# Optimization experiments

Measured on AMD Instinct MI355X. Metric: run time of the kernel, lower is better.

The kernel has to match this reference:

```python
import jax, jax.numpy as jnp
import numpy as np

K, N = 4, 128
NODEDIM = 256
EDGEDIM_IN = 256
EDGEDIM_OUT = 256
GLOBALDIM = 256
INFODIM = 2 * NODEDIM + GLOBALDIM + EDGEDIM_IN  # 1024


def setup_inputs() -> dict:
    key = jax.random.key(0)
    ks = jax.random.split(key, 10)
    u = jax.random.normal(ks[0], (K, GLOBALDIM), dtype=jnp.float32)
    h_v = jax.random.normal(ks[1], (K, N, NODEDIM), dtype=jnp.float32)
    h_e = jax.random.normal(ks[2], (K, N, N, EDGEDIM_IN), dtype=jnp.float32)
    V = jax.random.randint(ks[3], (K, N), 0, 2).astype(jnp.float32)  # binary node mask
    E = jax.random.randint(ks[4], (K, N, N, 2), 0, 2, dtype=jnp.int32)  # per-type edge mask
    # function[1] params (loop runs i in [1, num_functions) -> only i=1)
    s1 = 1.0 / np.sqrt(INFODIM)
    W1 = jax.random.uniform(ks[5], (INFODIM, INFODIM), jnp.float32, -s1, s1)
    b1 = jax.random.uniform(ks[6], (INFODIM,), jnp.float32, -s1, s1)
    W2 = jax.random.uniform(ks[7], (INFODIM, EDGEDIM_OUT), jnp.float32, -s1, s1)
    b2 = jax.random.uniform(ks[8], (EDGEDIM_OUT,), jnp.float32, -s1, s1)
    return {"u": u, "h_v": h_v, "h_e": h_e, "V": V, "E": E,
            "W1": W1, "b1": b1, "W2": W2, "b2": b2}


def reference(u, h_v, h_e, V, E, W1, b1, W2, b2):
    Kb, Nn = h_v.shape[0], h_v.shape[1]
    hv = h_v * V[..., None]                                    # masked node states
    src = jnp.broadcast_to(hv[:, :, None, :], (Kb, Nn, Nn, NODEDIM))
    tgt = jnp.broadcast_to(hv[:, None, :, :], (Kb, Nn, Nn, NODEDIM))
    glb = jnp.broadcast_to(u[:, None, None, :], (Kb, Nn, Nn, GLOBALDIM))
    edge_feat = jnp.concatenate([src, tgt, glb, h_e], axis=-1)  # [K,N,N,INFODIM]
    # per-type MLP (only function index 1 executes for num_functions=2)
    h = jax.nn.elu(jnp.einsum('knmi,ij->knmj', edge_feat, W1) + b1)
    out = jnp.einsum('knmi,io->knmo', h, W2) + b2               # [K,N,N,EDGEDIM_OUT]
    mask = (E[..., 1] == 1)[..., None]
    h_e_update = jnp.where(mask, out, jnp.zeros((), out.dtype))
    # residual=True, history=True
    return h_e_update + h_e
```

## Files before the change

### kernel.cpp

```cpp
#include <hip/hip_runtime.h>
#include <stdint.h>

#define DEVI __device__ __forceinline__

typedef short bf16x8 __attribute__((ext_vector_type(8)));
typedef float f32x4  __attribute__((ext_vector_type(4)));

DEVI short f2bf(float f){
  union { float f; uint32_t u; } un; un.f = f;
  uint32_t u = un.u;
  u += 0x7fffu + ((u >> 16) & 1u);
  return (short)(u >> 16);
}
DEVI float bf2f(uint32_t us){
  union { uint32_t u; float f; } x; x.u = us << 16; return x.f;
}

DEVI f32x4 mfma16(bf16x8 a, bf16x8 b, f32x4 c){
  return __builtin_amdgcn_mfma_f32_16x16x32_bf16(a, b, c, 0, 0, 0);
}

__global__ __launch_bounds__(256) void prep_all(
    const float* __restrict__ W1, const float* __restrict__ W2,
    const float* __restrict__ hv, const float* __restrict__ V,
    const float* __restrict__ u,
    short* __restrict__ w1t, short* __restrict__ w2t,
    short* __restrict__ hvb, short* __restrict__ ub)
{
  const int bid = blockIdx.x;
  if (bid < 1280){
    const float* W = (bid < 1024) ? W1 : W2;
    short* WT      = (bid < 1024) ? w1t : w2t;
    const int R = 1024;
    const int C = (bid < 1024) ? 1024 : 256;
    const int b2 = (bid < 1024) ? bid : (bid - 1024);
    __shared__ float tile[32][33];
    int ctiles = C >> 5;
    int bi = b2 / ctiles, bj = b2 % ctiles;
    int tx = threadIdx.x & 31, ty = threadIdx.x >> 5;
    #pragma unroll
    for (int r = 0; r < 4; ++r){
      int i = bi*32 + ty + r*8;
      tile[ty + r*8][tx] = W[(size_t)i*C + bj*32 + tx];
    }
    __syncthreads();
    #pragma unroll
    for (int r = 0; r < 4; ++r){
      int j = bj*32 + ty + r*8;
      WT[(size_t)j*R + bi*32 + tx] = f2bf(tile[tx][ty + r*8]);
    }
  } else {
    int idx = (bid - 1280)*256 + threadIdx.x;
    if (idx < 512*256){
      int r = idx >> 8;
      hvb[idx] = f2bf(hv[idx] * V[r]);
    } else if (idx < 512*256 + 1024){
      int i2 = idx - 512*256;
      ub[i2] = f2bf(u[i2]);
    }
  }
}

__global__ __launch_bounds__(256) void prep_st(
    const short* __restrict__ hvb, const short* __restrict__ ub,
    const short* __restrict__ w1t, const float* __restrict__ b1,
    short* __restrict__ sbuf, short* __restrict__ tbuf)
{
  const int bid = blockIdx.x;
  const int st = bid >> 7;
  const int rt8 = (bid >> 4) & 7;
  const int ctile = bid & 15;
  const int r0 = rt8 << 6, j0 = ctile << 6;
  const int tid = threadIdx.x;
  const int w = tid >> 6, l = tid & 63;
  const int l15 = l & 15, l4 = l >> 4;
  __shared__ short A[64*256];
  __shared__ short Stile[64][64];
  for (int q = 0; q < 8; ++q){
    int id = tid + (q << 8);
    int row = id >> 5, c8 = id & 31;
    bf16x8 v = *(const bf16x8*)(hvb + (size_t)(r0 + row)*256 + c8*8);
    *(bf16x8*)((char*)A + row*512 + ((c8*16) ^ ((row & 7) << 4))) = v;
  }
  __syncthreads();
  const int wr = w >> 1, wc = w & 1;
  const int rowbase = wr << 5, colbase = wc << 5;
  const int swzA = (l15 & 7) << 4;
  f32x4 acc[2][2];
  acc[0][0]=0; acc[0][1]=0; acc[1][0]=0; acc[1][1]=0;
  const int ioff = st ? 256 : 0;
  const short* w1p = w1t + (size_t)(j0 + colbase + l15)*1024 + ioff + l4*8;
  const char* ap0 = (const char*)A + (rowbase + l15)*512;
  const char* ap1 = ap0 + 16*512;
  #pragma unroll
  for (int kk = 0; kk < 8; ++kk){
    int ib = kk*64 + l4*16;
    bf16x8 a0 = *(const bf16x8*)(ap0 + (ib ^ swzA));
    bf16x8 a1 = *(const bf16x8*)(ap1 + (ib ^ swzA));
    bf16x8 b0 = *(const bf16x8*)(w1p + kk*32);
    bf16x8 b1v = *(const bf16x8*)(w1p + 16*1024 + kk*32);
    acc[0][0] = mfma16(a0, b0, acc[0][0]);
    acc[1][0] = mfma16(a1, b0, acc[1][0]);
    acc[0][1] = mfma16(a0, b1v, acc[0][1]);
    acc[1][1] = mfma16(a1, b1v, acc[1][1]);
  }
  if (st == 0){
    const int kb = r0 >> 7;
    const short* up = ub + kb*256 + l4*8;
    const short* w1pu = w1t + (size_t)(j0 + colbase + l15)*1024 + 512 + l4*8;
    #pragma unroll
    for (int kk = 0; kk < 8; ++kk){
      bf16x8 au = *(const bf16x8*)(up + kk*32);
      bf16x8 b0 = *(const bf16x8*)(w1pu + kk*32);
      bf16x8 b1v = *(const bf16x8*)(w1pu + 16*1024 + kk*32);
      acc[0][0] = mfma16(au, b0, acc[0][0]);
      acc[1][0] = mfma16(au, b0, acc[1][0]);
      acc[0][1] = mfma16(au, b1v, acc[0][1]);
      acc[1][1] = mfma16(au, b1v, acc[1][1]);
    }
  }
  #pragma unroll
  for (int r = 0; r < 2; ++r){
    #pragma unroll
    for (int c = 0; c < 2; ++c){
      int jl = colbase + c*16 + l15;
      float badd = st ? 0.f : b1[j0 + jl];
      #pragma unroll
      for (int reg = 0; reg < 4; ++reg){
        int rowl = rowbase + r*16 + l4*4 + reg;
        short v = f2bf(acc[r][c][reg] + badd);
        if (st == 0) Stile[rowl][jl] = v;
        else         Stile[jl][rowl] = v;
      }
    }
  }
  __syncthreads();
  {
    int a = tid >> 2, ch = (tid & 3) << 4;
    bf16x8 v0 = *(const bf16x8*)(&Stile[a][ch]);
    bf16x8 v1 = *(const bf16x8*)(&Stile[a][ch + 8]);
    short* dst = (st == 0)
      ? (sbuf + (size_t)(r0 + a)*1024 + j0 + ch)
      : (tbuf + (size_t)(j0 + a)*512  + r0 + ch);
    *(bf16x8*)(dst)     = v0;
    *(bf16x8*)(dst + 8) = v1;
  }
}

__global__ __launch_bounds__(512, 2) void fused_edge(
    const float* __restrict__ he, const unsigned short* __restrict__ sb,
    const unsigned short* __restrict__ tbT, const short* __restrict__ w1t,
    const short* __restrict__ w2t, const float* __restrict__ b2,
    const int* __restrict__ Em, float* __restrict__ out)
{
  const int bo = blockIdx.x;
  const int b = ((bo & 7) << 6) | (bo >> 3);
  const int kp = b >> 8;
  const int n  = (b >> 1) & 127;
  const int m0 = (b & 1) << 6;
  const int k0 = kp << 1;
  const int tid = threadIdx.x;
  const int w = tid >> 6, l = tid & 63;
  const int l15 = l & 15, l4 = l >> 4;

  __shared__ short heb[128*256];
  __shared__ short eluv[2][128*128];
  __shared__ int   emask[128];

  const int base0 = (k0*128 + n)*128 + m0;

  #pragma unroll
  for (int q = 0; q < 8; ++q){
    int id = tid + (q << 9);
    int row = id >> 5, c8 = id & 31;
    size_t grow = (size_t)base0 + (row >> 6)*16384 + (row & 63);
    const float4* p = (const float4*)(he + grow*256 + c8*8);
    float4 a4 = p[0], b4 = p[1];
    union { bf16x8 v; short s[8]; } pk;
    pk.s[0]=f2bf(a4.x); pk.s[1]=f2bf(a4.y); pk.s[2]=f2bf(a4.z); pk.s[3]=f2bf(a4.w);
    pk.s[4]=f2bf(b4.x); pk.s[5]=f2bf(b4.y); pk.s[6]=f2bf(b4.z); pk.s[7]=f2bf(b4.w);
    *(bf16x8*)((char*)heb + row*512 + ((c8*16) ^ ((row & 7) << 4))) = pk.v;
  }
  if (tid < 128)
    emask[tid] = Em[((size_t)base0 + (tid >> 6)*16384 + (tid & 63))*2 + 1];
  __syncthreads();

  f32x4 acc2[8][2];
  #pragma unroll
  for (int i = 0; i < 8; ++i){ acc2[i][0] = 0; acc2[i][1] = 0; }

  const unsigned short* srow0 = sb + (size_t)(k0*128 + n)*1024;
  const unsigned short* srow1 = srow0 + 128*1024;
  const int tcol0 = k0*128 + m0;
  const int tcol1 = tcol0 + 128;
  const char* hb = (const char*)heb;
  const int swz = (l15 & 7) << 4;

  union u4 { ushort4 v; unsigned short s[4]; };

  bf16x8 bw1[8];
  {
    const short* w1p = w1t + (size_t)(w*16 + l15)*1024 + 768 + l4*8;
    #pragma unroll
    for (int kk = 0; kk < 8; ++kk) bw1[kk] = *(const bf16x8*)(w1p + kk*32);
  }
  u4 t4[8];
  #pragma unroll
  for (int rt = 0; rt < 8; ++rt){
    int tc = (rt < 4) ? (tcol0 + rt*16) : (tcol1 + (rt - 4)*16);
    t4[rt].v = *(const ushort4*)(tbT + (size_t)(w*16 + l15)*512 + tc + l4*4);
  }
  float sv0 = bf2f(srow0[w*16 + l15]);
  float sv1 = bf2f(srow1[w*16 + l15]);

  for (int ph = 0; ph < 8; ++ph){
    const int jcol = ph*128 + w*16 + l15;

    f32x4 acc1[8];
    #pragma unroll
    for (int i = 0; i < 8; ++i) acc1[i] = 0;
    #pragma unroll
    for (int kk = 0; kk < 8; ++kk){
      int ib = kk*64 + l4*16;
      #pragma unroll
      for (int rt = 0; rt < 8; ++rt){
        int row = rt*16 + l15;
        bf16x8 a = *(const bf16x8*)(hb + row*512 + (ib ^ swz));
        acc1[rt] = mfma16(a, bw1[kk], acc1[rt]);
      }
    }

    const short* w2p = w2t + (size_t)(w*32 + l15)*1024 + ph*128 + l4*8;
    bf16x8 bw2[2][4];
    #pragma unroll
    for (int ct = 0; ct < 2; ++ct)
      #pragma unroll
      for (int kk = 0; kk < 4; ++kk)
        bw2[ct][kk] = *(const bf16x8*)(w2p + (size_t)ct*16*1024 + kk*32);

    if (ph < 7){
      const short* w1p = w1t + (size_t)(jcol + 128)*1024 + 768 + l4*8;
      #pragma unroll
      for (int kk = 0; kk < 8; ++kk) bw1[kk] = *(const bf16x8*)(w1p + kk*32);
    }

    char* eb = (char*)(&eluv[ph & 1][0]);
    const int cb = (w*16 + l15)*2;
    #pragma unroll
    for (int rt = 0; rt < 8; ++rt){
      float sv = (rt < 4) ? sv0 : sv1;
      #pragma unroll
      for (int reg = 0; reg < 4; ++reg){
        int row = rt*16 + l4*4 + reg;
        float v = acc1[rt][reg] + sv + bf2f(t4[rt].s[reg]);
        v = v > 0.f ? v : (__expf(v) - 1.f);
        *(short*)(eb + row*256 + (cb ^ ((row & 7) << 4))) = f2bf(v);
      }
    }

    if (ph < 7){
      #pragma unroll
      for (int rt = 0; rt < 8; ++rt){
        int tc = (rt < 4) ? (tcol0 + rt*16) : (tcol1 + (rt - 4)*16);
        t4[rt].v = *(const ushort4*)(tbT + (size_t)(jcol + 128)*512 + tc + l4*4);
      }
      sv0 = bf2f(srow0[jcol + 128]);
      sv1 = bf2f(srow1[jcol + 128]);
    }
    __syncthreads();

    #pragma unroll
    for (int kk = 0; kk < 4; ++kk){
      int jb = kk*64 + l4*16;
      #pragma unroll
      for (int rt = 0; rt < 8; ++rt){
        int row = rt*16 + l15;
        bf16x8 a2 = *(const bf16x8*)(eb + row*256 + (jb ^ ((row & 7) << 4)));
        acc2[rt][0] = mfma16(a2, bw2[0][kk], acc2[rt][0]);
        acc2[rt][1] = mfma16(a2, bw2[1][kk], acc2[rt][1]);
      }
    }
  }

  const float bias0 = b2[w*32 + l15];
  const float bias1 = b2[w*32 + 16 + l15];
  #pragma unroll
  for (int rt = 0; rt < 8; ++rt){
    #pragma unroll
    for (int reg = 0; reg < 4; ++reg){
      int row = rt*16 + l4*4 + reg;
      int e = emask[row];
      size_t grow = (size_t)base0 + (row >> 6)*16384 + (row & 63);
      float* op = out + grow*256 + w*32 + l15;
      const char* hrow = hb + row*512;
      int sw = (row & 7) << 4;
      float hv0 = bf2f(*(const unsigned short*)(hrow + (((w*32 + l15)*2) ^ sw)));
      float hv1 = bf2f(*(const unsigned short*)(hrow + (((w*32 + 16 + l15)*2) ^ sw)));
      op[0]  = ((e == 1) ? (acc2[rt][0][reg] + bias0) : 0.f) + hv0;
      op[16] = ((e == 1) ? (acc2[rt][1][reg] + bias1) : 0.f) + hv1;
    }
  }
}

extern "C" void kernel_launch(void* const* d_in, const int* in_sizes, int n_in,
                              void* d_out, int out_size, void* d_ws, size_t ws_size,
                              hipStream_t stream)
{
  const float* u   = (const float*)d_in[0];
  const float* h_v = (const float*)d_in[1];
  const float* h_e = (const float*)d_in[2];
  const float* V   = (const float*)d_in[3];
  const int*   E   = (const int*)d_in[4];
  const float* W1  = (const float*)d_in[5];
  const float* b1  = (const float*)d_in[6];
  const float* W2  = (const float*)d_in[7];
  const float* b2  = (const float*)d_in[8];
  float* out = (float*)d_out;

  char* ws = (char*)d_ws;
  short* w1t  = (short*)(ws);
  short* w2t  = (short*)(ws + (2u<<20));
  short* hvb  = (short*)(ws + (2u<<20) + (512u<<10));
  short* ub   = (short*)(ws + (2u<<20) + (768u<<10));
  short* sbuf = (short*)(ws + (3u<<20));
  short* tbuf = (short*)(ws + (4u<<20));

  prep_all<<<1796, 256, 0, stream>>>(W1, W2, h_v, V, u, w1t, w2t, hvb, ub);
  prep_st<<<256, 256, 0, stream>>>(hvb, ub, w1t, b1, sbuf, tbuf);
  fused_edge<<<512, 512, 0, stream>>>(h_e,
                                      (const unsigned short*)sbuf,
                                      (const unsigned short*)tbuf,
                                      w1t, w2t, b2, E, out);
}
```

Measured before the change: 177.0 us.

## Process two hidden column tiles per phase with single ELU buffer

Each warp now computes two 16-column slices of the first GEMM per phase (256 hidden columns), so every LDS read of the edge-feature A fragment feeds two MFMAs, and the phase count halves from 8 to 4. The double-buffered ELU tile is replaced by a single 128x256 buffer with an extra barrier before it is overwritten. Weight fragments are now loaded inside the k-loop instead of being prefetched a phase ahead. Register pressure roughly doubles for the layer-1 accumulators, which risks spills under the 512x2 launch bounds, and the second barrier plus the loss of weight prefetch may expose load latency.

```diff
diff --git a/kernel.cpp b/kernel.cpp
--- a/kernel.cpp
+++ b/kernel.cpp
@@ -164,7 +164,7 @@
   const int l15 = l & 15, l4 = l >> 4;
 
   __shared__ short heb[128*256];
-  __shared__ short eluv[2][128*128];
+  __shared__ short eluv[128*256];
   __shared__ int   emask[128];
 
   const int base0 = (k0*128 + n)*128 + m0;
@@ -194,90 +194,94 @@
   const int tcol0 = k0*128 + m0;
   const int tcol1 = tcol0 + 128;
   const char* hb = (const char*)heb;
+  const char* eb = (const char*)eluv;
   const int swz = (l15 & 7) << 4;
 
   union u4 { ushort4 v; unsigned short s[4]; };
 
-  bf16x8 bw1[8];
-  {
-    const short* w1p = w1t + (size_t)(w*16 + l15)*1024 + 768 + l4*8;
-    #pragma unroll
-    for (int kk = 0; kk < 8; ++kk) bw1[kk] = *(const bf16x8*)(w1p + kk*32);
-  }
-  u4 t4[8];
+  u4 t4a[8], t4b[8];
   #pragma unroll
   for (int rt = 0; rt < 8; ++rt){
     int tc = (rt < 4) ? (tcol0 + rt*16) : (tcol1 + (rt - 4)*16);
-    t4[rt].v = *(const ushort4*)(tbT + (size_t)(w*16 + l15)*512 + tc + l4*4);
-  }
-  float sv0 = bf2f(srow0[w*16 + l15]);
-  float sv1 = bf2f(srow1[w*16 + l15]);
-
-  for (int ph = 0; ph < 8; ++ph){
-    const int jcol = ph*128 + w*16 + l15;
-
-    f32x4 acc1[8];
-    #pragma unroll
-    for (int i = 0; i < 8; ++i) acc1[i] = 0;
-    #pragma unroll
-    for (int kk = 0; kk < 8; ++kk){
-      int ib = kk*64 + l4*16;
-      #pragma unroll
-      for (int rt = 0; rt < 8; ++rt){
-        int row = rt*16 + l15;
-        bf16x8 a = *(const bf16x8*)(hb + row*512 + (ib ^ swz));
-        acc1[rt] = mfma16(a, bw1[kk], acc1[rt]);
-      }
-    }
-
-    const short* w2p = w2t + (size_t)(w*32 + l15)*1024 + ph*128 + l4*8;
-    bf16x8 bw2[2][4];
-    #pragma unroll
-    for (int ct = 0; ct < 2; ++ct)
-      #pragma unroll
-      for (int kk = 0; kk < 4; ++kk)
-        bw2[ct][kk] = *(const bf16x8*)(w2p + (size_t)ct*16*1024 + kk*32);
-
-    if (ph < 7){
-      const short* w1p = w1t + (size_t)(jcol + 128)*1024 + 768 + l4*8;
-      #pragma unroll
-      for (int kk = 0; kk < 8; ++kk) bw1[kk] = *(const bf16x8*)(w1p + kk*32);
-    }
-
-    char* eb = (char*)(&eluv[ph & 1][0]);
-    const int cb = (w*16 + l15)*2;
+    t4a[rt].v = *(const ushort4*)(tbT + (size_t)(w*16 + l15)*512       + tc + l4*4);
+    t4b[rt].v = *(const ushort4*)(tbT + (size_t)(w*16 + l15 + 128)*512 + tc + l4*4);
+  }
+  float sva0 = bf2f(srow0[w*16 + l15]),       sva1 = bf2f(srow1[w*16 + l15]);
+  float svb0 = bf2f(srow0[w*16 + l15 + 128]), svb1 = bf2f(srow1[w*16 + l15 + 128]);
+
+  for (int ph = 0; ph < 4; ++ph){
+    const int jca = ph*256 + w*16 + l15;
+    const int jcb = jca + 128;
+
+    f32x4 acc1a[8], acc1b[8];
+    #pragma unroll
+    for (int i = 0; i < 8; ++i){ acc1a[i] = 0; acc1b[i] = 0; }
+    {
+      const short* wpa = w1t + (size_t)jca*1024 + 768 + l4*8;
+      const short* wpb = w1t + (size_t)jcb*1024 + 768 + l4*8;
+      #pragma unroll
+      for (int kk = 0; kk < 8; ++kk){
+        bf16x8 ba = *(const bf16x8*)(wpa + kk*32);
+        bf16x8 bb = *(const bf16x8*)(wpb + kk*32);
+        int ib = kk*64 + l4*16;
+        #pragma unroll
+        for (int rt = 0; rt < 8; ++rt){
+          int row = rt*16 + l15;
+          bf16x8 a = *(const bf16x8*)(hb + row*512 + (ib ^ swz));
+          acc1a[rt] = mfma16(a, ba, acc1a[rt]);
+          acc1b[rt] = mfma16(a, bb, acc1b[rt]);
+        }
+      }
+    }
+
+    __syncthreads();
+
+    const int cba = (w*16 + l15)*2;
+    const int cbb = cba + 256;
     #pragma unroll
     for (int rt = 0; rt < 8; ++rt){
-      float sv = (rt < 4) ? sv0 : sv1;
+      float sa = (rt < 4) ? sva0 : sva1;
+      float sbv = (rt < 4) ? svb0 : svb1;
       #pragma unroll
       for (int reg = 0; reg < 4; ++reg){
         int row = rt*16 + l4*4 + reg;
-        float v = acc1[rt][reg] + sv + bf2f(t4[rt].s[reg]);
-        v = v > 0.f ? v : (__expf(v) - 1.f);
-        *(short*)(eb + row*256 + (cb ^ ((row & 7) << 4))) = f2bf(v);
-      }
-    }
-
-    if (ph < 7){
+        int sw = (row & 7) << 4;
+        float va = acc1a[rt][reg] + sa + bf2f(t4a[rt].s[reg]);
+        float vb = acc1b[rt][reg] + sbv + bf2f(t4b[rt].s[reg]);
+        va = va > 0.f ? va : (__expf(va) - 1.f);
+        vb = vb > 0.f ? vb : (__expf(vb) - 1.f);
+        *(short*)((char*)eluv + row*512 + (cba ^ sw)) = f2bf(va);
+        *(short*)((char*)eluv + row*512 + (cbb ^ sw)) = f2bf(vb);
+      }
+    }
+
+    if (ph < 3){
       #pragma unroll
       for (int rt = 0; rt < 8; ++rt){
         int tc = (rt < 4) ? (tcol0 + rt*16) : (tcol1 + (rt - 4)*16);
-        t4[rt].v = *(const ushort4*)(tbT + (size_t)(jcol + 128)*512 + tc + l4*4);
-      }
-      sv0 = bf2f(srow0[jcol + 128]);
-      sv1 = bf2f(srow1[jcol + 128]);
+        t4a[rt].v = *(const ushort4*)(tbT + (size_t)(jca + 256)*512 + tc + l4*4);
+        t4b[rt].v = *(const ushort4*)(tbT + (size_t)(jcb + 256)*512 + tc + l4*4);
+      }
+      sva0 = bf2f(srow0[jca + 256]); sva1 = bf2f(srow1[jca + 256]);
+      svb0 = bf2f(srow0[jcb + 256]); svb1 = bf2f(srow1[jcb + 256]);
     }
     __syncthreads();
 
-    #pragma unroll
-    for (int kk = 0; kk < 4; ++kk){
-      int jb = kk*64 + l4*16;
-      #pragma unroll
-      for (int rt = 0; rt < 8; ++rt){
-        int row = rt*16 + l15;
-        bf16x8 a2 = *(const bf16x8*)(eb + row*256 + (jb ^ ((row & 7) << 4)));
-        acc2[rt][0] = mfma16(a2, bw2[0][kk], acc2[rt][0]);
-        acc2[rt][1] = mfma16(a2, bw2[1][kk], acc2[rt][1]);
+    {
+      const short* wpa = w2t + (size_t)(w*32 + l15)*1024      + ph*256 + l4*8;
+      const short* wpb = w2t + (size_t)(w*32 + 16 + l15)*1024 + ph*256 + l4*8;
+      #pragma unroll
+      for (int kk = 0; kk < 8; ++kk){
+        bf16x8 ba = *(const bf16x8*)(wpa + kk*32);
+        bf16x8 bb = *(const bf16x8*)(wpb + kk*32);
+        int jb = kk*64 + l4*16;
+        #pragma unroll
+        for (int rt = 0; rt < 8; ++rt){
+          int row = rt*16 + l15;
+          bf16x8 a2 = *(const bf16x8*)(eb + row*512 + (jb ^ swz));
+          acc2[rt][0] = mfma16(a2, ba, acc2[rt][0]);
+          acc2[rt][1] = mfma16(a2, bb, acc2[rt][1]);
+        }
       }
     }
   }
```

Result: slower. 209.1 us (+18.1%).

## Retile first GEMM warps to 64x32 blocks for A-fragment reuse

Applied to the files above, without the earlier changes.

Changes the per-warp tiling of the first GEMM from 128 rows by 16 columns to 64 rows by 32 columns, so each LDS A-fragment load feeds two MFMAs. Each warp now handles a single k-batch half, which removes the per-tile selection between two srow/tcol sources. The goal is to halve the LDS reads per MFMA in the hidden-layer GEMM. In exchange each warp holds twice as many W1 fragments in registers.

```diff
diff --git a/kernel.cpp b/kernel.cpp
--- a/kernel.cpp
+++ b/kernel.cpp
@@ -189,44 +189,50 @@
   #pragma unroll
   for (int i = 0; i < 8; ++i){ acc2[i][0] = 0; acc2[i][1] = 0; }
 
-  const unsigned short* srow0 = sb + (size_t)(k0*128 + n)*1024;
-  const unsigned short* srow1 = srow0 + 128*1024;
-  const int tcol0 = k0*128 + m0;
-  const int tcol1 = tcol0 + 128;
+  const int rowbase = (w & 1) << 6;
+  const int colg    = (w >> 1) << 5;
+  const int myk     = w & 1;
+  const unsigned short* srow = sb + (size_t)((k0 + myk)*128 + n)*1024;
+  const int tcol = (k0 + myk)*128 + m0;
   const char* hb = (const char*)heb;
   const int swz = (l15 & 7) << 4;
 
   union u4 { ushort4 v; unsigned short s[4]; };
 
-  bf16x8 bw1[8];
+  bf16x8 bw1a[8], bw1b[8];
   {
-    const short* w1p = w1t + (size_t)(w*16 + l15)*1024 + 768 + l4*8;
-    #pragma unroll
-    for (int kk = 0; kk < 8; ++kk) bw1[kk] = *(const bf16x8*)(w1p + kk*32);
-  }
-  u4 t4[8];
-  #pragma unroll
-  for (int rt = 0; rt < 8; ++rt){
-    int tc = (rt < 4) ? (tcol0 + rt*16) : (tcol1 + (rt - 4)*16);
-    t4[rt].v = *(const ushort4*)(tbT + (size_t)(w*16 + l15)*512 + tc + l4*4);
-  }
-  float sv0 = bf2f(srow0[w*16 + l15]);
-  float sv1 = bf2f(srow1[w*16 + l15]);
+    const short* w1pa = w1t + (size_t)(colg + l15)*1024 + 768 + l4*8;
+    #pragma unroll
+    for (int kk = 0; kk < 8; ++kk){
+      bw1a[kk] = *(const bf16x8*)(w1pa + kk*32);
+      bw1b[kk] = *(const bf16x8*)(w1pa + 16*1024 + kk*32);
+    }
+  }
+  u4 t4a[4], t4b[4];
+  #pragma unroll
+  for (int rt = 0; rt < 4; ++rt){
+    t4a[rt].v = *(const ushort4*)(tbT + (size_t)(colg + l15)*512      + tcol + rt*16 + l4*4);
+    t4b[rt].v = *(const ushort4*)(tbT + (size_t)(colg + 16 + l15)*512 + tcol + rt*16 + l4*4);
+  }
+  float sva = bf2f(srow[colg + l15]);
+  float svb = bf2f(srow[colg + 16 + l15]);
 
   for (int ph = 0; ph < 8; ++ph){
-    const int jcol = ph*128 + w*16 + l15;
-
-    f32x4 acc1[8];
-    #pragma unroll
-    for (int i = 0; i < 8; ++i) acc1[i] = 0;
+    const int jca = ph*128 + colg + l15;
+
+    f32x4 acc1[4][2];
+    #pragma unroll
+    for (int i = 0; i < 4; ++i){ acc1[i][0] = 0; acc1[i][1] = 0; }
     #pragma unroll
     for (int kk = 0; kk < 8; ++kk){
       int ib = kk*64 + l4*16;
-      #pragma unroll
-      for (int rt = 0; rt < 8; ++rt){
-        int row = rt*16 + l15;
+      bf16x8 ba = bw1a[kk], bb = bw1b[kk];
+      #pragma unroll
+      for (int rt = 0; rt < 4; ++rt){
+        int row = rowbase + rt*16 + l15;
         bf16x8 a = *(const bf16x8*)(hb + row*512 + (ib ^ swz));
-        acc1[rt] = mfma16(a, bw1[kk], acc1[rt]);
+        acc1[rt][0] = mfma16(a, ba, acc1[rt][0]);
+        acc1[rt][1] = mfma16(a, bb, acc1[rt][1]);
       }
     }
 
@@ -239,33 +245,39 @@
         bw2[ct][kk] = *(const bf16x8*)(w2p + (size_t)ct*16*1024 + kk*32);
 
     if (ph < 7){
-      const short* w1p = w1t + (size_t)(jcol + 128)*1024 + 768 + l4*8;
-      #pragma unroll
-      for (int kk = 0; kk < 8; ++kk) bw1[kk] = *(const bf16x8*)(w1p + kk*32);
+      const short* w1pa = w1t + (size_t)(jca + 128)*1024 + 768 + l4*8;
+      #pragma unroll
+      for (int kk = 0; kk < 8; ++kk){
+        bw1a[kk] = *(const bf16x8*)(w1pa + kk*32);
+        bw1b[kk] = *(const bf16x8*)(w1pa + 16*1024 + kk*32);
+      }
     }
 
     char* eb = (char*)(&eluv[ph & 1][0]);
-    const int cb = (w*16 + l15)*2;
-    #pragma unroll
-    for (int rt = 0; rt < 8; ++rt){
-      float sv = (rt < 4) ? sv0 : sv1;
+    const int cba = (colg + l15)*2;
+    #pragma unroll
+    for (int rt = 0; rt < 4; ++rt){
       #pragma unroll
       for (int reg = 0; reg < 4; ++reg){
-        int row = rt*16 + l4*4 + reg;
-        float v = acc1[rt][reg] + sv + bf2f(t4[rt].s[reg]);
-        v = v > 0.f ? v : (__expf(v) - 1.f);
-        *(short*)(eb + row*256 + (cb ^ ((row & 7) << 4))) = f2bf(v);
+        int row = rowbase + rt*16 + l4*4 + reg;
+        int sw = (row & 7) << 4;
+        float va = acc1[rt][0][reg] + sva + bf2f(t4a[rt].s[reg]);
+        float vb = acc1[rt][1][reg] + svb + bf2f(t4b[rt].s[reg]);
+        va = va > 0.f ? va : (__expf(va) - 1.f);
+        vb = vb > 0.f ? vb : (__expf(vb) - 1.f);
+        *(short*)(eb + row*256 + (cba ^ sw))        = f2bf(va);
+        *(short*)(eb + row*256 + ((cba + 32) ^ sw)) = f2bf(vb);
       }
     }
 
     if (ph < 7){
       #pragma unroll
-      for (int rt = 0; rt < 8; ++rt){
-        int tc = (rt < 4) ? (tcol0 + rt*16) : (tcol1 + (rt - 4)*16);
-        t4[rt].v = *(const ushort4*)(tbT + (size_t)(jcol + 128)*512 + tc + l4*4);
-      }
-      sv0 = bf2f(srow0[jcol + 128]);
-      sv1 = bf2f(srow1[jcol + 128]);
+      for (int rt = 0; rt < 4; ++rt){
+        t4a[rt].v = *(const ushort4*)(tbT + (size_t)(jca + 128)*512      + tcol + rt*16 + l4*4);
+        t4b[rt].v = *(const ushort4*)(tbT + (size_t)(jca + 16 + 128)*512 + tcol + rt*16 + l4*4);
+      }
+      sva = bf2f(srow[jca + 128]);
+      svb = bf2f(srow[jca + 16 + 128]);
     }
     __syncthreads();
 
```

Measured after the change: 220.8 us. +24.7%, slower.

## Double fused_edge block to 1024 threads and split work across 16 waves

Applied to the files above, without the earlier changes.

The fused edge kernel now runs 16 waves per block instead of 8. In the first GEMM each wave handles a 16-column group for half the rows, one k-slice each. In the second GEMM each wave owns 16 output columns instead of 32. The goal is more waves per CU to hide memory and LDS latency, since the LDS footprint already limits residency to one block per CU. In exchange, pairs of waves load the same W1 fragments, and the launch_bounds(1024,4) setting may force a very tight register budget, which could cause spills.

```diff
diff --git a/kernel.cpp b/kernel.cpp
--- a/kernel.cpp
+++ b/kernel.cpp
@@ -147,7 +147,7 @@
   }
 }
 
-__global__ __launch_bounds__(512, 2) void fused_edge(
+__global__ __launch_bounds__(1024, 4) void fused_edge(
     const float* __restrict__ he, const unsigned short* __restrict__ sb,
     const unsigned short* __restrict__ tbT, const short* __restrict__ w1t,
     const short* __restrict__ w2t, const float* __restrict__ b2,
@@ -170,8 +170,8 @@
   const int base0 = (k0*128 + n)*128 + m0;
 
   #pragma unroll
-  for (int q = 0; q < 8; ++q){
-    int id = tid + (q << 9);
+  for (int q = 0; q < 4; ++q){
+    int id = tid + (q << 10);
     int row = id >> 5, c8 = id & 31;
     size_t grow = (size_t)base0 + (row >> 6)*16384 + (row & 63);
     const float4* p = (const float4*)(he + grow*256 + c8*8);
@@ -185,14 +185,15 @@
     emask[tid] = Em[((size_t)base0 + (tid >> 6)*16384 + (tid & 63))*2 + 1];
   __syncthreads();
 
-  f32x4 acc2[8][2];
-  #pragma unroll
-  for (int i = 0; i < 8; ++i){ acc2[i][0] = 0; acc2[i][1] = 0; }
-
-  const unsigned short* srow0 = sb + (size_t)(k0*128 + n)*1024;
-  const unsigned short* srow1 = srow0 + 128*1024;
-  const int tcol0 = k0*128 + m0;
-  const int tcol1 = tcol0 + 128;
+  f32x4 acc2[8];
+  #pragma unroll
+  for (int i = 0; i < 8; ++i) acc2[i] = 0;
+
+  const int rowbase = (w & 1) << 6;
+  const int colg    = (w >> 1) << 4;
+  const int myk     = w & 1;
+  const unsigned short* srow = sb + (size_t)((k0 + myk)*128 + n)*1024;
+  const int tcol = (k0 + myk)*128 + m0;
   const char* hb = (const char*)heb;
   const int swz = (l15 & 7) << 4;
 
@@ -200,43 +201,37 @@
 
   bf16x8 bw1[8];
   {
-    const short* w1p = w1t + (size_t)(w*16 + l15)*1024 + 768 + l4*8;
+    const short* w1p = w1t + (size_t)(colg + l15)*1024 + 768 + l4*8;
     #pragma unroll
     for (int kk = 0; kk < 8; ++kk) bw1[kk] = *(const bf16x8*)(w1p + kk*32);
   }
-  u4 t4[8];
-  #pragma unroll
-  for (int rt = 0; rt < 8; ++rt){
-    int tc = (rt < 4) ? (tcol0 + rt*16) : (tcol1 + (rt - 4)*16);
-    t4[rt].v = *(const ushort4*)(tbT + (size_t)(w*16 + l15)*512 + tc + l4*4);
-  }
-  float sv0 = bf2f(srow0[w*16 + l15]);
-  float sv1 = bf2f(srow1[w*16 + l15]);
+  u4 t4[4];
+  #pragma unroll
+  for (int rt = 0; rt < 4; ++rt)
+    t4[rt].v = *(const ushort4*)(tbT + (size_t)(colg + l15)*512 + tcol + rt*16 + l4*4);
+  float sv = bf2f(srow[colg + l15]);
 
   for (int ph = 0; ph < 8; ++ph){
-    const int jcol = ph*128 + w*16 + l15;
-
-    f32x4 acc1[8];
-    #pragma unroll
-    for (int i = 0; i < 8; ++i) acc1[i] = 0;
+    const int jcol = ph*128 + colg + l15;
+
+    f32x4 acc1[4];
+    acc1[0]=0; acc1[1]=0; acc1[2]=0; acc1[3]=0;
     #pragma unroll
     for (int kk = 0; kk < 8; ++kk){
       int ib = kk*64 + l4*16;
       #pragma unroll
-      for (int rt = 0; rt < 8; ++rt){
-        int row = rt*16 + l15;
+      for (int rt = 0; rt < 4; ++rt){
+        int row = rowbase + rt*16 + l15;
         bf16x8 a = *(const bf16x8*)(hb + row*512 + (ib ^ swz));
         acc1[rt] = mfma16(a, bw1[kk], acc1[rt]);
       }
     }
 
-    const short* w2p = w2t + (size_t)(w*32 + l15)*1024 + ph*128 + l4*8;
-    bf16x8 bw2[2][4];
-    #pragma unroll
-    for (int ct = 0; ct < 2; ++ct)
-      #pragma unroll
-      for (int kk = 0; kk < 4; ++kk)
-        bw2[ct][kk] = *(const bf16x8*)(w2p + (size_t)ct*16*1024 + kk*32);
+    const short* w2p = w2t + (size_t)(w*16 + l15)*1024 + ph*128 + l4*8;
+    bf16x8 bw2[4];
+    #pragma unroll
+    for (int kk = 0; kk < 4; ++kk)
+      bw2[kk] = *(const bf16x8*)(w2p + kk*32);
 
     if (ph < 7){
       const short* w1p = w1t + (size_t)(jcol + 128)*1024 + 768 + l4*8;
@@ -245,13 +240,12 @@
     }
 
     char* eb = (char*)(&eluv[ph & 1][0]);
-    const int cb = (w*16 + l15)*2;
-    #pragma unroll
-    for (int rt = 0; rt < 8; ++rt){
-      float sv = (rt < 4) ? sv0 : sv1;
+    const int cb = (colg + l15)*2;
+    #pragma unroll
+    for (int rt = 0; rt < 4; ++rt){
       #pragma unroll
       for (int reg = 0; reg < 4; ++reg){
-        int row = rt*16 + l4*4 + reg;
+        int row = rowbase + rt*16 + l4*4 + reg;
         float v = acc1[rt][reg] + sv + bf2f(t4[rt].s[reg]);
         v = v > 0.f ? v : (__expf(v) - 1.f);
         *(short*)(eb + row*256 + (cb ^ ((row & 7) << 4))) = f2bf(v);
@@ -260,12 +254,9 @@
 
     if (ph < 7){
       #pragma unroll
-      for (int rt = 0; rt < 8; ++rt){
-        int tc = (rt < 4) ? (tcol0 + rt*16) : (tcol1 + (rt - 4)*16);
-        t4[rt].v = *(const ushort4*)(tbT + (size_t)(jcol + 128)*512 + tc + l4*4);
-      }
-      sv0 = bf2f(srow0[jcol + 128]);
-      sv1 = bf2f(srow1[jcol + 128]);
+      for (int rt = 0; rt < 4; ++rt)
+        t4[rt].v = *(const ushort4*)(tbT + (size_t)(jcol + 128)*512 + tcol + rt*16 + l4*4);
+      sv = bf2f(srow[jcol + 128]);
     }
     __syncthreads();
 
@@ -276,14 +267,12 @@
       for (int rt = 0; rt < 8; ++rt){
         int row = rt*16 + l15;
         bf16x8 a2 = *(const bf16x8*)(eb + row*256 + (jb ^ ((row & 7) << 4)));
-        acc2[rt][0] = mfma16(a2, bw2[0][kk], acc2[rt][0]);
-        acc2[rt][1] = mfma16(a2, bw2[1][kk], acc2[rt][1]);
+        acc2[rt] = mfma16(a2, bw2[kk], acc2[rt]);
       }
     }
   }
 
-  const float bias0 = b2[w*32 + l15];
-  const float bias1 = b2[w*32 + 16 + l15];
+  const float bias = b2[w*16 + l15];
   #pragma unroll
   for (int rt = 0; rt < 8; ++rt){
     #pragma unroll
@@ -291,13 +280,11 @@
       int row = rt*16 + l4*4 + reg;
       int e = emask[row];
       size_t grow = (size_t)base0 + (row >> 6)*16384 + (row & 63);
-      float* op = out + grow*256 + w*32 + l15;
+      float* op = out + grow*256 + w*16 + l15;
       const char* hrow = hb + row*512;
       int sw = (row & 7) << 4;
-      float hv0 = bf2f(*(const unsigned short*)(hrow + (((w*32 + l15)*2) ^ sw)));
-      float hv1 = bf2f(*(const unsigned short*)(hrow + (((w*32 + 16 + l15)*2) ^ sw)));
-      op[0]  = ((e == 1) ? (acc2[rt][0][reg] + bias0) : 0.f) + hv0;
-      op[16] = ((e == 1) ? (acc2[rt][1][reg] + bias1) : 0.f) + hv1;
+      float hv = bf2f(*(const unsigned short*)(hrow + (((w*16 + l15)*2) ^ sw)));
+      op[0] = ((e == 1) ? (acc2[rt][reg] + bias) : 0.f) + hv;
     }
   }
 }
@@ -327,8 +314,8 @@
 
   prep_all<<<1796, 256, 0, stream>>>(W1, W2, h_v, V, u, w1t, w2t, hvb, ub);
   prep_st<<<256, 256, 0, stream>>>(hvb, ub, w1t, b1, sbuf, tbuf);
-  fused_edge<<<512, 512, 0, stream>>>(h_e,
-                                      (const unsigned short*)sbuf,
-                                      (const unsigned short*)tbuf,
-                                      w1t, w2t, b2, E, out);
-}
+  fused_edge<<<512, 1024, 0, stream>>>(h_e,
+                                       (const unsigned short*)sbuf,
+                                       (const unsigned short*)tbuf,
+                                       w1t, w2t, b2, E, out);
+}
```

Result: slower. 218.6 us (+23.5%).
